# Kernel tuning notes

Measured on AMD Instinct MI355X. Metric: run time of the kernel, lower is better.

The kernel has to match this reference:

```python
import jax, jax.numpy as jnp
import numpy as np

DIM = 512
HEADS = 8        # MultiHeadAttention default heads=8 (init 'heads' arg actually sets dim_head)
DIM_HEAD = 64    # from AttentionLayers heads=64 passed positionally as dim_head
HIDDEN = HEADS * DIM_HEAD  # 512
EPS = 1e-5


def setup_inputs() -> dict:
    key = jax.random.key(0)
    ks = jax.random.split(key, 8)
    s = 1.0 / np.sqrt(DIM)
    return {
        "x": jax.random.normal(ks[0], (4, 2048, DIM), dtype=jnp.float32),
        "ln_g": jnp.ones((DIM,), dtype=jnp.float32),
        "ln_b": jnp.zeros((DIM,), dtype=jnp.float32),
        "Wq": jax.random.normal(ks[1], (DIM, HIDDEN), dtype=jnp.float32) * s,
        "Wk": jax.random.normal(ks[2], (DIM, HIDDEN), dtype=jnp.float32) * s,
        "Wv": jax.random.normal(ks[3], (DIM, HIDDEN), dtype=jnp.float32) * s,
        "Wo": jax.random.normal(ks[4], (HIDDEN, DIM), dtype=jnp.float32) * s,
        "bo": jnp.zeros((DIM,), dtype=jnp.float32),
    }


def reference(x, ln_g, ln_b, Wq, Wk, Wv, Wo, bo):
    b, n, d = x.shape
    residual = x
    # pre-norm LayerNorm
    mu = jnp.mean(x, axis=-1, keepdims=True)
    var = jnp.mean((x - mu) ** 2, axis=-1, keepdims=True)
    xn = (x - mu) * jax.lax.rsqrt(var + EPS) * ln_g + ln_b
    # QKV projections (no bias), split into heads: [b, s, h, dh]
    q = (xn @ Wq).reshape(b, n, HEADS, DIM_HEAD)
    k = (xn @ Wk).reshape(b, n, HEADS, DIM_HEAD)
    v = (xn @ Wv).reshape(b, n, HEADS, DIM_HEAD)
    scale = HIDDEN ** (-0.5)  # note: scales by hidden_dim, not dim_head (faithful)
    scores = jnp.einsum('bihd,bjhd->bhij', q, k) * scale  # [b,h,i,j] full matrix
    attn = jax.nn.softmax(scores, axis=-1)
    out = jnp.einsum('bhij,bjhd->bihd', attn, v).reshape(b, n, HIDDEN)
    out = out @ Wo + bo
    # residual; the subsequent FFN layer's output is discarded in the source
    return out + residual
```

## Files before the change

kernel.cpp:

```cpp
#include <hip/hip_runtime.h>
#include <hip/hip_bf16.h>

#define DIM 512
#define SEQ 2048
#define BATCH 4
#define NHEADS 8
#define DH 64
#define NROWS (BATCH * SEQ)
#define LN_EPS 1e-5f

typedef __hip_bfloat16 bf16;
typedef __attribute__((ext_vector_type(8))) short short8;
typedef __attribute__((ext_vector_type(4))) float f32x4;

#define MFMA16(a, b, c) __builtin_amdgcn_mfma_f32_16x16x32_bf16((a), (b), (c), 0, 0, 0)

#if __has_builtin(__builtin_amdgcn_exp2f)
#define EXP2(x) __builtin_amdgcn_exp2f(x)
#else
#define EXP2(x) exp2f(x)
#endif

#if defined(__has_builtin)
#if __has_builtin(__builtin_amdgcn_global_load_lds)
#define HAS_GLDS 1
#endif
#endif

__device__ __forceinline__ void glds16(const bf16* g, bf16* l) {
#ifdef HAS_GLDS
  __builtin_amdgcn_global_load_lds((const __attribute__((address_space(1))) void*)g,
                                   (__attribute__((address_space(3))) void*)l, 16, 0, 0);
#else
  *reinterpret_cast<uint4*>(l) = *reinterpret_cast<const uint4*>(g);
#endif
}

__device__ __forceinline__ void store_bf16x4(bf16* p, float a, float b, float c, float d) {
  bf16 tmp[4] = {__float2bfloat16(a), __float2bfloat16(b), __float2bfloat16(c),
                 __float2bfloat16(d)};
  *reinterpret_cast<ushort4*>(p) = *reinterpret_cast<const ushort4*>(tmp);
}

#define B2F(us) __uint_as_float(((unsigned)(us)) << 16)

#define Q_SCALE_LOG2E 0.06375872f

__global__ void setup_kernel(const float* __restrict__ x, const float* __restrict__ gamma,
                             const float* __restrict__ beta, bf16* __restrict__ xn,
                             const float* __restrict__ Wq, const float* __restrict__ Wk,
                             const float* __restrict__ Wv, const float* __restrict__ Wo,
                             bf16* __restrict__ Wt) {
  __shared__ float red[8];
  __shared__ float stats[2];
  __shared__ float tile[32][33];
  const int t = threadIdx.x;
  if (blockIdx.x < NROWS) {
    const int row = blockIdx.x;
    const float2 v = reinterpret_cast<const float2*>(x + (size_t)row * DIM)[t];
    float s = v.x + v.y;
    float ss = v.x * v.x + v.y * v.y;
#pragma unroll
    for (int off = 32; off > 0; off >>= 1) {
      s += __shfl_down(s, off);
      ss += __shfl_down(ss, off);
    }
    if ((t & 63) == 0) { red[(t >> 6) * 2] = s; red[(t >> 6) * 2 + 1] = ss; }
    __syncthreads();
    if (t == 0) {
      float S = red[0] + red[2] + red[4] + red[6];
      float SS = red[1] + red[3] + red[5] + red[7];
      float mu = S * (1.0f / DIM);
      float var = SS * (1.0f / DIM) - mu * mu;
      stats[0] = mu;
      stats[1] = rsqrtf(var + LN_EPS);
    }
    __syncthreads();
    const float mu = stats[0], rs = stats[1];
    const float2 gg = reinterpret_cast<const float2*>(gamma)[t];
    const float2 bb = reinterpret_cast<const float2*>(beta)[t];
    __hip_bfloat162 o;
    o.x = __float2bfloat16((v.x - mu) * rs * gg.x + bb.x);
    o.y = __float2bfloat16((v.y - mu) * rs * gg.y + bb.y);
    reinterpret_cast<__hip_bfloat162*>(xn + (size_t)row * DIM)[t] = o;
  } else {
    const int idx = blockIdx.x - NROWS;
    const int bx = idx & 15, by = (idx >> 4) & 15, z = idx >> 8;
    const float* __restrict__ W = (z == 0) ? Wq : (z == 1) ? Wk : (z == 2) ? Wv : Wo;
    const float scale = (z == 0) ? Q_SCALE_LOG2E : 1.0f;
    bf16* __restrict__ dst = Wt + (size_t)z * DIM * DIM;
    const int tx = t & 31, ty = t >> 5;
#pragma unroll
    for (int i = 0; i < 32; i += 8)
      tile[ty + i][tx] = W[(size_t)(by * 32 + ty + i) * DIM + bx * 32 + tx];
    __syncthreads();
#pragma unroll
    for (int i = 0; i < 32; i += 8)
      dst[(size_t)(bx * 32 + ty + i) * DIM + by * 32 + tx] =
          __float2bfloat16(tile[tx][ty + i] * scale);
  }
}

__launch_bounds__(256, 3)
__global__ void gemm_qkv_kernel(const bf16* __restrict__ A, const bf16* __restrict__ Bt,
                                bf16* __restrict__ qo, bf16* __restrict__ ko,
                                bf16* __restrict__ vto) {
  const int m0 = blockIdx.x * 128, n0g = blockIdx.y * 128;
  __shared__ __align__(16) char smem[128 * 136 * 2];
  bf16* const sA = (bf16*)smem;
  bf16* const sB = (bf16*)(smem + 16384);
  bf16* const sT = (bf16*)smem;
  const int t = threadIdx.x, w = t >> 6, l = t & 63;
  const int r = l & 15, g = l >> 4;
  const int wm = w >> 1, wn = w & 1;
  const int crow = w * 32 + (l >> 2);
  const int ccol = (l & 3) * 8;
  const bf16* gA = A + (size_t)(m0 + crow) * DIM + ccol;
  const bf16* gB = Bt + (size_t)(n0g + crow) * DIM + ccol;
  const int loff = w * 1024 + l * 8;
  f32x4 acc[4][4] = {};
  glds16(gA, sA + loff);
  glds16(gA + 16 * DIM, sA + loff + 512);
  glds16(gB, sB + loff);
  glds16(gB + 16 * DIM, sB + loff + 512);
  const int NK = DIM / 32;
  for (int ks = 0; ks < NK; ks++) {
    const int cur = ks & 1;
    __syncthreads();
    if (ks + 1 < NK) {
      const int k0n = (ks + 1) * 32;
      glds16(gA + k0n, sA + (1 - cur) * 4096 + loff);
      glds16(gA + 16 * DIM + k0n, sA + (1 - cur) * 4096 + loff + 512);
      glds16(gB + k0n, sB + (1 - cur) * 4096 + loff);
      glds16(gB + 16 * DIM + k0n, sB + (1 - cur) * 4096 + loff + 512);
    }
    short8 af[4], bfv[4];
#pragma unroll
    for (int i = 0; i < 4; i++)
      af[i] = *reinterpret_cast<const short8*>(
          &sA[cur * 4096 + (wm * 64 + i * 16 + r) * 32 + g * 8]);
#pragma unroll
    for (int j = 0; j < 4; j++)
      bfv[j] = *reinterpret_cast<const short8*>(
          &sB[cur * 4096 + (wn * 64 + j * 16 + r) * 32 + g * 8]);
#pragma unroll
    for (int i = 0; i < 4; i++)
#pragma unroll
      for (int j = 0; j < 4; j++) acc[i][j] = MFMA16(af[i], bfv[j], acc[i][j]);
  }
  const int z = n0g >> 9;
  const int b = m0 / SEQ;
  if (z != 2) {
    bf16* __restrict__ outp = (z == 0) ? qo : ko;
    const int nc0 = (n0g & 511) + wn * 64;
#pragma unroll
    for (int i = 0; i < 4; i++)
#pragma unroll
      for (int j = 0; j < 4; j++)
#pragma unroll
        for (int reg = 0; reg < 4; reg++) {
          const int m = m0 + wm * 64 + i * 16 + g * 4 + reg;
          const int col = nc0 + j * 16 + r;
          outp[(size_t)m * DIM + col] = __float2bfloat16(acc[i][j][reg]);
        }
  } else {
    __syncthreads();
#pragma unroll
    for (int i = 0; i < 4; i++)
#pragma unroll
      for (int j = 0; j < 4; j++)
        store_bf16x4(&sT[(wn * 64 + j * 16 + r) * 136 + wm * 64 + i * 16 + g * 4],
                     acc[i][j][0], acc[i][j][1], acc[i][j][2], acc[i][j][3]);
    __syncthreads();
    const int dr = t >> 1;
    const int mc = (t & 1) * 64;
    const int dcol = (n0g & 511) + dr;
    bf16* dst = vto + ((size_t)b * DIM + dcol) * SEQ + (m0 - b * SEQ) + mc;
#pragma unroll
    for (int uu = 0; uu < 8; uu++)
      *reinterpret_cast<uint4*>(dst + uu * 8) =
          *reinterpret_cast<const uint4*>(&sT[dr * 136 + mc + uu * 8]);
  }
}

template <bool SPLIT>
__launch_bounds__(128, 3)
__global__ void attn_kernel(const bf16* __restrict__ q, const bf16* __restrict__ k,
                            const bf16* __restrict__ vt, bf16* __restrict__ opart,
                            float* __restrict__ lpart) {
  const int it = blockIdx.x, bh = blockIdx.y, jh = blockIdx.z;
  const int b = bh >> 3, h = bh & 7;
  const int t = threadIdx.x, wv = t >> 6, l = t & 63;
  const int r = l & 15, g = l >> 4;
  __shared__ __align__(16) bf16 sK[64 * 64];
  __shared__ __align__(16) bf16 sV[64 * 64];
  __shared__ __align__(16) bf16 sPt[2][2][16][72];
  const int i0 = it * 64 + wv * 32;
  const bf16* qp = q + ((size_t)(b * SEQ) + i0 + r) * DIM + h * DH;
  short8 qf[2][2];
#pragma unroll
  for (int s = 0; s < 2; s++)
#pragma unroll
    for (int kc = 0; kc < 2; kc++)
      qf[s][kc] = *reinterpret_cast<const short8*>(qp + s * 16 * DIM + kc * 32 + g * 8);
  f32x4 oacc[2][4] = {};
  float lsum[2] = {0.f, 0.f};
  const int jbase = SPLIT ? jh * (SEQ / 2) : 0;
  const int srow8 = l >> 3;
  const int u = ((l & 7) - srow8) & 7;
  const bf16* kg = k + ((size_t)(b * SEQ) + jbase + wv * 32 + srow8) * DIM + h * DH + u * 8;
  const bf16* vg = vt + ((size_t)(b * DIM) + h * DH + wv * 32 + srow8) * SEQ + jbase + u * 8;
  const int loff = wv * 2048 + l * 8;
  const int e0 = 64 * r + 8 * ((g + r) & 7);
  const int e1 = 64 * r + 8 * ((4 + g + r) & 7);
  const int NJ = SPLIT ? (SEQ / 2) / 64 : SEQ / 64;
  for (int jt = 0; jt < NJ; jt++) {
    const int j0 = jt * 64;
#pragma unroll
    for (int cc = 0; cc < 4; cc++) {
      glds16(kg + (size_t)(j0 + cc * 8) * DIM, sK + loff + cc * 512);
      glds16(vg + (size_t)(cc * 8) * SEQ + j0, sV + loff + cc * 512);
    }
    __syncthreads();
    f32x4 st[2][4];
#pragma unroll
    for (int c = 0; c < 4; c++) {
      const short8 kf0 = *reinterpret_cast<const short8*>(sK + 1024 * c + e0);
      const short8 kf1 = *reinterpret_cast<const short8*>(sK + 1024 * c + e1);
#pragma unroll
      for (int s = 0; s < 2; s++) {
        f32x4 a = {0.f, 0.f, 0.f, 0.f};
        a = MFMA16(kf0, qf[s][0], a);
        a = MFMA16(kf1, qf[s][1], a);
        st[s][c] = a;
      }
    }
#pragma unroll
    for (int s = 0; s < 2; s++)
#pragma unroll
      for (int c = 0; c < 4; c++) {
        const float p0 = EXP2(st[s][c][0]);
        const float p1 = EXP2(st[s][c][1]);
        const float p2 = EXP2(st[s][c][2]);
        const float p3 = EXP2(st[s][c][3]);
        lsum[s] += (p0 + p1) + (p2 + p3);
        store_bf16x4(&sPt[wv][s][r][c * 16 + g * 4], p0, p1, p2, p3);
      }
#pragma unroll
    for (int kc2 = 0; kc2 < 2; kc2++) {
      short8 pf[2];
#pragma unroll
      for (int s = 0; s < 2; s++)
        pf[s] = *reinterpret_cast<const short8*>(&sPt[wv][s][r][kc2 * 32 + g * 8]);
      const int ev = (kc2 == 0) ? e0 : e1;
#pragma unroll
      for (int dt = 0; dt < 4; dt++) {
        const short8 vf = *reinterpret_cast<const short8*>(sV + 1024 * dt + ev);
#pragma unroll
        for (int s = 0; s < 2; s++) oacc[s][dt] = MFMA16(vf, pf[s], oacc[s][dt]);
      }
    }
    __syncthreads();
  }
#pragma unroll
  for (int s = 0; s < 2; s++) {
    lsum[s] += __shfl_xor(lsum[s], 16);
    lsum[s] += __shfl_xor(lsum[s], 32);
  }
  const size_t obase = ((size_t)(SPLIT ? jh * 32 : 0) + bh) * SEQ;
#pragma unroll
  for (int s = 0; s < 2; s++) {
    const int i = i0 + s * 16 + r;
    if (l < 16) lpart[obase + i] = lsum[s];
#pragma unroll
    for (int dt = 0; dt < 4; dt++)
      store_bf16x4(opart + (obase + i) * 64 + dt * 16 + g * 4, oacc[s][dt][0], oacc[s][dt][1],
                   oacc[s][dt][2], oacc[s][dt][3]);
  }
  if (!SPLIT) {
    const size_t obase1 = ((size_t)32 + bh) * SEQ;
#pragma unroll
    for (int s = 0; s < 2; s++) {
      const int i = i0 + s * 16 + r;
      if (l < 16) lpart[obase1 + i] = 0.f;
#pragma unroll
      for (int dt = 0; dt < 4; dt++)
        store_bf16x4(opart + (obase1 + i) * 64 + dt * 16 + g * 4, 0.f, 0.f, 0.f, 0.f);
    }
  }
}

__launch_bounds__(256, 2)
__global__ void gemm_proj_kernel(const bf16* __restrict__ opart, const float* __restrict__ lpart,
                                 const bf16* __restrict__ Bt, const float* __restrict__ bo,
                                 const float* __restrict__ x, float* __restrict__ out) {
  const int m0 = blockIdx.x * 128, n0 = blockIdx.y * 64;
  __shared__ __align__(16) bf16 sA[128 * 32];
  __shared__ __align__(16) bf16 sB[64 * 32];
  const int t = threadIdx.x, w = t >> 6, l = t & 63;
  const int r = l & 15, g = l >> 4;
  const int wm = w >> 1, wn = w & 1;
  const int arow = t >> 2;
  const int acol = (t & 3) * 8;
  const bf16* gB = Bt + (size_t)(n0 + arow) * DIM + acol;
  f32x4 acc[4][2] = {};
  const int NK = DIM / 32;
  for (int ks = 0; ks < NK; ks++) {
    const int k0 = ks * 32;
    const int h = k0 >> 6;
    const int d0 = (k0 & 63) + acol;
    uint4 areg[2];
#pragma unroll
    for (int c = 0; c < 2; c++) {
      const int m = m0 + c * 64 + arow;
      const int bb = m >> 11, ii = m & 2047;
      const size_t row0 = ((size_t)(bb * 8 + h)) * SEQ + ii;
      const size_t row1 = row0 + (size_t)32 * SEQ;
      const uint4 A0 = *reinterpret_cast<const uint4*>(opart + row0 * 64 + d0);
      const uint4 A1 = *reinterpret_cast<const uint4*>(opart + row1 * 64 + d0);
      const float inv = 1.0f / (lpart[row0] + lpart[row1]);
      const ushort* a0 = (const ushort*)&A0;
      const ushort* a1 = (const ushort*)&A1;
      bf16 rr[8];
#pragma unroll
      for (int e = 0; e < 8; e++)
        rr[e] = __float2bfloat16((B2F(a0[e]) + B2F(a1[e])) * inv);
      areg[c] = *reinterpret_cast<const uint4*>(rr);
    }
    const uint4 breg = *reinterpret_cast<const uint4*>(gB + k0);
    __syncthreads();
    *reinterpret_cast<uint4*>(&sA[(0 * 64 + arow) * 32 + acol]) = areg[0];
    *reinterpret_cast<uint4*>(&sA[(1 * 64 + arow) * 32 + acol]) = areg[1];
    *reinterpret_cast<uint4*>(&sB[arow * 32 + acol]) = breg;
    __syncthreads();
    short8 af[4], bfv[2];
#pragma unroll
    for (int i = 0; i < 4; i++)
      af[i] = *reinterpret_cast<const short8*>(&sA[(wm * 64 + i * 16 + r) * 32 + g * 8]);
#pragma unroll
    for (int j = 0; j < 2; j++)
      bfv[j] = *reinterpret_cast<const short8*>(&sB[(wn * 32 + j * 16 + r) * 32 + g * 8]);
#pragma unroll
    for (int i = 0; i < 4; i++)
#pragma unroll
      for (int j = 0; j < 2; j++) acc[i][j] = MFMA16(af[i], bfv[j], acc[i][j]);
  }
#pragma unroll
  for (int i = 0; i < 4; i++)
#pragma unroll
    for (int j = 0; j < 2; j++)
#pragma unroll
      for (int reg = 0; reg < 4; reg++) {
        const int m = m0 + wm * 64 + i * 16 + g * 4 + reg;
        const int col = n0 + wn * 32 + j * 16 + r;
        out[(size_t)m * DIM + col] = acc[i][j][reg] + bo[col] + x[(size_t)m * DIM + col];
      }
}

extern "C" void kernel_launch(void* const* d_in, const int* in_sizes, int n_in,
                              void* d_out, int out_size, void* d_ws, size_t ws_size,
                              hipStream_t stream) {
  (void)in_sizes; (void)n_in; (void)out_size;
  const float* x    = (const float*)d_in[0];
  const float* ln_g = (const float*)d_in[1];
  const float* ln_b = (const float*)d_in[2];
  const float* Wq   = (const float*)d_in[3];
  const float* Wk   = (const float*)d_in[4];
  const float* Wv   = (const float*)d_in[5];
  const float* Wo   = (const float*)d_in[6];
  const float* bo   = (const float*)d_in[7];
  float* out = (float*)d_out;
  char* ws = (char*)d_ws;
  bf16* xn  = (bf16*)(ws);
  bf16* wt  = (bf16*)(ws + (8u << 20));
  bf16* qb  = (bf16*)(ws + (10u << 20));
  bf16* kb  = (bf16*)(ws + (18u << 20));
  bf16* vtb = (bf16*)(ws + (26u << 20));
  bf16* opart = (bf16*)(ws + (34u << 20));
  float* lpart = (float*)(ws + (50u << 20));
  const bool split = ws_size >= ((50u << 20) + (1u << 19));

  setup_kernel<<<NROWS + 1024, 256, 0, stream>>>(x, ln_g, ln_b, xn, Wq, Wk, Wv, Wo, wt);
  gemm_qkv_kernel<<<dim3(NROWS / 128, (3 * DIM) / 128), 256, 0, stream>>>(xn, wt, qb, kb, vtb);
  if (split) {
    attn_kernel<true><<<dim3(SEQ / 64, BATCH * NHEADS, 2), 128, 0, stream>>>(
        qb, kb, vtb, opart, lpart);
  } else {
    attn_kernel<false><<<dim3(SEQ / 64, BATCH * NHEADS, 1), 128, 0, stream>>>(
        qb, kb, vtb, opart, lpart);
  }
  gemm_proj_kernel<<<dim3(NROWS / 128, DIM / 64), 256, 0, stream>>>(
      opart, lpart, wt + 3 * DIM * DIM, bo, x, out);
}
```

Baseline: 179.7 us.

## Widen attention blocks to 4 waves sharing K/V tiles; pack 4 LayerNorm rows per block

```diff
diff --git a/kernel.cpp b/kernel.cpp
--- a/kernel.cpp
+++ b/kernel.cpp
@@ -51,40 +51,35 @@
                              const float* __restrict__ Wq, const float* __restrict__ Wk,
                              const float* __restrict__ Wv, const float* __restrict__ Wo,
                              bf16* __restrict__ Wt) {
-  __shared__ float red[8];
-  __shared__ float stats[2];
-  __shared__ float tile[32][33];
   const int t = threadIdx.x;
-  if (blockIdx.x < NROWS) {
-    const int row = blockIdx.x;
-    const float2 v = reinterpret_cast<const float2*>(x + (size_t)row * DIM)[t];
-    float s = v.x + v.y;
-    float ss = v.x * v.x + v.y * v.y;
-#pragma unroll
-    for (int off = 32; off > 0; off >>= 1) {
-      s += __shfl_down(s, off);
-      ss += __shfl_down(ss, off);
-    }
-    if ((t & 63) == 0) { red[(t >> 6) * 2] = s; red[(t >> 6) * 2 + 1] = ss; }
-    __syncthreads();
-    if (t == 0) {
-      float S = red[0] + red[2] + red[4] + red[6];
-      float SS = red[1] + red[3] + red[5] + red[7];
-      float mu = S * (1.0f / DIM);
-      float var = SS * (1.0f / DIM) - mu * mu;
-      stats[0] = mu;
-      stats[1] = rsqrtf(var + LN_EPS);
-    }
-    __syncthreads();
-    const float mu = stats[0], rs = stats[1];
-    const float2 gg = reinterpret_cast<const float2*>(gamma)[t];
-    const float2 bb = reinterpret_cast<const float2*>(beta)[t];
-    __hip_bfloat162 o;
-    o.x = __float2bfloat16((v.x - mu) * rs * gg.x + bb.x);
-    o.y = __float2bfloat16((v.y - mu) * rs * gg.y + bb.y);
-    reinterpret_cast<__hip_bfloat162*>(xn + (size_t)row * DIM)[t] = o;
+  if (blockIdx.x < NROWS / 4) {
+    const int row = blockIdx.x * 4 + (t >> 6);
+    const int l = t & 63;
+    const float4* xr = reinterpret_cast<const float4*>(x + (size_t)row * DIM);
+    const float4 v0 = xr[l * 2];
+    const float4 v1 = xr[l * 2 + 1];
+    float s = (v0.x + v0.y + v0.z + v0.w) + (v1.x + v1.y + v1.z + v1.w);
+    float ss = v0.x * v0.x + v0.y * v0.y + v0.z * v0.z + v0.w * v0.w + v1.x * v1.x +
+               v1.y * v1.y + v1.z * v1.z + v1.w * v1.w;
+#pragma unroll
+    for (int off = 1; off < 64; off <<= 1) {
+      s += __shfl_xor(s, off);
+      ss += __shfl_xor(ss, off);
+    }
+    const float mu = s * (1.0f / DIM);
+    const float rs = rsqrtf(ss * (1.0f / DIM) - mu * mu + LN_EPS);
+    const float4 g0 = reinterpret_cast<const float4*>(gamma)[l * 2];
+    const float4 g1 = reinterpret_cast<const float4*>(gamma)[l * 2 + 1];
+    const float4 b0 = reinterpret_cast<const float4*>(beta)[l * 2];
+    const float4 b1 = reinterpret_cast<const float4*>(beta)[l * 2 + 1];
+    bf16* o = xn + (size_t)row * DIM + l * 8;
+    store_bf16x4(o, (v0.x - mu) * rs * g0.x + b0.x, (v0.y - mu) * rs * g0.y + b0.y,
+                 (v0.z - mu) * rs * g0.z + b0.z, (v0.w - mu) * rs * g0.w + b0.w);
+    store_bf16x4(o + 4, (v1.x - mu) * rs * g1.x + b1.x, (v1.y - mu) * rs * g1.y + b1.y,
+                 (v1.z - mu) * rs * g1.z + b1.z, (v1.w - mu) * rs * g1.w + b1.w);
   } else {
-    const int idx = blockIdx.x - NROWS;
+    __shared__ float tile[32][33];
+    const int idx = blockIdx.x - NROWS / 4;
     const int bx = idx & 15, by = (idx >> 4) & 15, z = idx >> 8;
     const float* __restrict__ W = (z == 0) ? Wq : (z == 1) ? Wk : (z == 2) ? Wv : Wo;
     const float scale = (z == 0) ? Q_SCALE_LOG2E : 1.0f;
@@ -184,18 +179,18 @@
 }
 
 template <bool SPLIT>
-__launch_bounds__(128, 3)
+__launch_bounds__(256, 4)
 __global__ void attn_kernel(const bf16* __restrict__ q, const bf16* __restrict__ k,
                             const bf16* __restrict__ vt, bf16* __restrict__ opart,
                             float* __restrict__ lpart) {
-  const int it = blockIdx.x, bh = blockIdx.y, jh = blockIdx.z;
+  const int bh = blockIdx.x, jh = blockIdx.y, it = blockIdx.z;
   const int b = bh >> 3, h = bh & 7;
   const int t = threadIdx.x, wv = t >> 6, l = t & 63;
   const int r = l & 15, g = l >> 4;
   __shared__ __align__(16) bf16 sK[64 * 64];
   __shared__ __align__(16) bf16 sV[64 * 64];
-  __shared__ __align__(16) bf16 sPt[2][2][16][72];
-  const int i0 = it * 64 + wv * 32;
+  __shared__ __align__(16) bf16 sPt[4][2][16][72];
+  const int i0 = it * 128 + wv * 32;
   const bf16* qp = q + ((size_t)(b * SEQ) + i0 + r) * DIM + h * DH;
   short8 qf[2][2];
 #pragma unroll
@@ -208,16 +203,16 @@
   const int jbase = SPLIT ? jh * (SEQ / 2) : 0;
   const int srow8 = l >> 3;
   const int u = ((l & 7) - srow8) & 7;
-  const bf16* kg = k + ((size_t)(b * SEQ) + jbase + wv * 32 + srow8) * DIM + h * DH + u * 8;
-  const bf16* vg = vt + ((size_t)(b * DIM) + h * DH + wv * 32 + srow8) * SEQ + jbase + u * 8;
-  const int loff = wv * 2048 + l * 8;
+  const bf16* kg = k + ((size_t)(b * SEQ) + jbase + wv * 16 + srow8) * DIM + h * DH + u * 8;
+  const bf16* vg = vt + ((size_t)(b * DIM) + h * DH + wv * 16 + srow8) * SEQ + jbase + u * 8;
+  const int loff = wv * 1024 + l * 8;
   const int e0 = 64 * r + 8 * ((g + r) & 7);
   const int e1 = 64 * r + 8 * ((4 + g + r) & 7);
   const int NJ = SPLIT ? (SEQ / 2) / 64 : SEQ / 64;
   for (int jt = 0; jt < NJ; jt++) {
     const int j0 = jt * 64;
 #pragma unroll
-    for (int cc = 0; cc < 4; cc++) {
+    for (int cc = 0; cc < 2; cc++) {
       glds16(kg + (size_t)(j0 + cc * 8) * DIM, sK + loff + cc * 512);
       glds16(vg + (size_t)(cc * 8) * SEQ + j0, sV + loff + cc * 512);
     }
@@ -380,13 +375,13 @@
   float* lpart = (float*)(ws + (50u << 20));
   const bool split = ws_size >= ((50u << 20) + (1u << 19));
 
-  setup_kernel<<<NROWS + 1024, 256, 0, stream>>>(x, ln_g, ln_b, xn, Wq, Wk, Wv, Wo, wt);
+  setup_kernel<<<NROWS / 4 + 1024, 256, 0, stream>>>(x, ln_g, ln_b, xn, Wq, Wk, Wv, Wo, wt);
   gemm_qkv_kernel<<<dim3(NROWS / 128, (3 * DIM) / 128), 256, 0, stream>>>(xn, wt, qb, kb, vtb);
   if (split) {
-    attn_kernel<true><<<dim3(SEQ / 64, BATCH * NHEADS, 2), 128, 0, stream>>>(
+    attn_kernel<true><<<dim3(BATCH * NHEADS, 2, SEQ / 128), 256, 0, stream>>>(
         qb, kb, vtb, opart, lpart);
   } else {
-    attn_kernel<false><<<dim3(SEQ / 64, BATCH * NHEADS, 1), 128, 0, stream>>>(
+    attn_kernel<false><<<dim3(BATCH * NHEADS, 1, SEQ / 128), 256, 0, stream>>>(
         qb, kb, vtb, opart, lpart);
   }
   gemm_proj_kernel<<<dim3(NROWS / 128, DIM / 64), 256, 0, stream>>>(
```

New measurement: 165.3 us. -8.0%, faster.
